# Kernel optimization log

Hardware: AMD Instinct MI355X
Metric: run time of the kernel (lower is better)

## Reference

```python
import jax, jax.numpy as jnp
import numpy as np

B, S, H, D = 2, 2048, 32, 128


def setup_inputs() -> dict:
    key = jax.random.key(0)
    qkv = jax.random.normal(key, (B, S, 3, H, D), dtype=jnp.float32)
    return {"qkv": qkv, "causal": 1}


def reference(qkv, causal):
    # qkv: [B, S, 3, H, D] packed as in flash_attn qkvpacked convention.
    # Distributed all-to-all / ring rotation is identity math on one device,
    # so this is standard scaled-dot-product attention.
    q = qkv[:, :, 0]  # [B, S, H, D]
    k = qkv[:, :, 1]
    v = qkv[:, :, 2]
    scale = 1.0 / jnp.sqrt(jnp.asarray(q.shape[-1], q.dtype))
    # [B, H, S, S]
    logits = jnp.einsum("bshd,bthd->bhst", q, k) * scale
    if causal:
        s = q.shape[1]
        mask = jnp.tril(jnp.ones((s, s), dtype=bool))  # [S, S]
        logits = jnp.where(mask[None, None], logits, jnp.finfo(logits.dtype).min)
    probs = jax.nn.softmax(logits, axis=-1)
    out = jnp.einsum("bhst,bthd->bshd", probs, v)  # [B, S, H, D]
    return out
```

## Files before the change

### kernel.cpp

```cpp
#include <hip/hip_runtime.h>
#include <hip/hip_bf16.h>

constexpr int Bc = 2;
constexpr int Sc = 2048;
constexpr int Hc = 32;
constexpr int Dc = 128;
constexpr int QKV_STRIDE = 3 * Hc * Dc;

constexpr int BQ = 128;
constexpr int BK = 64;
constexpr float SCALE_LOG2E = 0.088388347648318f * 1.442695040888963f;
constexpr float DEFER_THR = 8.0f;

constexpr int KST = 132;
constexpr int VST = 68;

typedef __attribute__((ext_vector_type(8)))  short    bf16x8;
typedef __attribute__((ext_vector_type(4)))  short    bf16x4;
typedef __attribute__((ext_vector_type(16))) float    f32x16;
typedef __attribute__((ext_vector_type(4)))  unsigned u32x4;

static __device__ __forceinline__ short f2bf(float f) {
    __bf16 h = (__bf16)f;
    return __builtin_bit_cast(short, h);
}
static __device__ __forceinline__ unsigned pk2(float lo, float hi) {
    union { short2 s; unsigned u; } x;
    x.s.x = f2bf(lo); x.s.y = f2bf(hi);
    return x.u;
}
static __device__ __forceinline__ void plswap(unsigned& dst, unsigned& src) {
    asm volatile("v_permlane32_swap_b32 %0, %1" : "+v"(dst), "+v"(src));
}
static __device__ __forceinline__ void lds_barrier() {
    asm volatile("s_waitcnt lgkmcnt(0)" ::: "memory");
    __builtin_amdgcn_s_barrier();
    asm volatile("" ::: "memory");
}

__global__ __launch_bounds__(256)
void attn_fwd(const float* __restrict__ qkv,
              const int* __restrict__ causal_p,
              float* __restrict__ out)
{
    const int bid = blockIdx.x;
    const int o   = bid >> 6;
    const int bh  = bid & 63;
    const int r_  = o & 3;
    const int j_  = o >> 2;
    const int bq_ = 15 - 2 * r_;
    const int qt  = (j_ < 2) ? (bq_ - j_) : (15 - bq_ + 3 - j_);

    const int b = bh >> 5;
    const int h = bh & 31;
    const int causal = *causal_p;

    const int tid  = threadIdx.x;
    const int w    = tid >> 6;
    const int lane = tid & 63;
    const int l31  = lane & 31;
    const int hf   = lane >> 5;

    __shared__ short Ks[64 * KST];
    __shared__ short Vs[128 * VST];

    const int q0  = qt * BQ;
    const int wq0 = q0 + w * 32;

    const int kg = tid >> 5;
    const int dl = tid & 31;

    const float* kplane = qkv + (size_t)b * Sc * QKV_STRIDE + Hc * Dc + h * Dc;

    bf16x8 qf[8];
    {
        const float* qb = qkv + (size_t)(b * Sc + wq0 + l31) * QKV_STRIDE + h * Dc;
        #pragma unroll
        for (int st = 0; st < 8; ++st) {
            const float* p = qb + st * 16 + hf * 8;
            float4 x0 = *(const float4*)(p);
            float4 x1 = *(const float4*)(p + 4);
            bf16x8 q;
            q[0] = f2bf(x0.x * SCALE_LOG2E);
            q[1] = f2bf(x0.y * SCALE_LOG2E);
            q[2] = f2bf(x0.z * SCALE_LOG2E);
            q[3] = f2bf(x0.w * SCALE_LOG2E);
            q[4] = f2bf(x1.x * SCALE_LOG2E);
            q[5] = f2bf(x1.y * SCALE_LOG2E);
            q[6] = f2bf(x1.z * SCALE_LOG2E);
            q[7] = f2bf(x1.w * SCALE_LOG2E);
            qf[st] = q;
        }
    }

    f32x16 o_[4];
    #pragma unroll
    for (int db = 0; db < 4; ++db)
        #pragma unroll
        for (int i = 0; i < 16; ++i) o_[db][i] = 0.f;
    float m = -1e30f, l = 0.f;

    const int nkv = causal ? (2 * qt + 2) : (Sc / BK);

    float4 kst[8];
    float  vst[8][4];

    auto issue = [&](int kt) {
        const float* kb = kplane + (size_t)(kt * BK + kg * 8) * QKV_STRIDE;
        #pragma unroll
        for (int j = 0; j < 8; ++j)
            kst[j] = *(const float4*)(kb + (size_t)j * QKV_STRIDE + dl * 4);
        const float* vb = kb + Hc * Dc;
        #pragma unroll
        for (int j = 0; j < 8; ++j) {
            #pragma unroll
            for (int q = 0; q < 4; ++q)
                vst[j][q] = vb[(size_t)j * QKV_STRIDE + q * 32 + dl];
        }
    };

    auto commit = [&]() {
        #pragma unroll
        for (int j = 0; j < 8; ++j) {
            bf16x4 kk;
            kk[0] = f2bf(kst[j].x); kk[1] = f2bf(kst[j].y);
            kk[2] = f2bf(kst[j].z); kk[3] = f2bf(kst[j].w);
            *(bf16x4*)&Ks[(kg * 8 + j) * KST + dl * 4] = kk;
        }
        #pragma unroll
        for (int q = 0; q < 4; ++q) {
            bf16x8 vv;
            #pragma unroll
            for (int j = 0; j < 8; ++j) vv[j] = f2bf(vst[j][q]);
            *(bf16x8*)&Vs[(q * 32 + dl) * VST + kg * 8] = vv;
        }
    };

    issue(0);

    for (int kt = 0; kt < nkv; ++kt) {
        lds_barrier();
        commit();
        if (kt + 1 < nkv) issue(kt + 1);
        lds_barrier();

        const int kbase = kt * BK;
        if (causal && kbase > wq0 + 31) continue;

        f32x16 acc[2];
        #pragma unroll
        for (int mb = 0; mb < 2; ++mb)
            #pragma unroll
            for (int i = 0; i < 16; ++i) acc[mb][i] = 0.f;
        __builtin_amdgcn_s_setprio(1);
        #pragma unroll
        for (int st = 0; st < 8; ++st) {
            #pragma unroll
            for (int mb = 0; mb < 2; ++mb) {
                bf16x8 ka = *(const bf16x8*)&Ks[(mb * 32 + l31) * KST + st * 16 + hf * 8];
                acc[mb] = __builtin_amdgcn_mfma_f32_32x32x16_bf16(ka, qf[st], acc[mb], 0, 0, 0);
            }
        }
        __builtin_amdgcn_s_setprio(0);

        if (causal && kbase + 63 > wq0) {
            const int qg = wq0 + l31;
            #pragma unroll
            for (int mb = 0; mb < 2; ++mb) {
                #pragma unroll
                for (int r = 0; r < 16; ++r) {
                    const int kgl = kbase + mb * 32 + (r & 3) + 8 * (r >> 2) + 4 * hf;
                    if (kgl > qg) acc[mb][r] = -1e30f;
                }
            }
        }

        float pm = acc[0][0];
        #pragma unroll
        for (int i = 1; i < 16; ++i) pm = fmaxf(pm, acc[0][i]);
        #pragma unroll
        for (int i = 0; i < 16; ++i) pm = fmaxf(pm, acc[1][i]);
        pm = fmaxf(pm, __shfl_xor(pm, 32));
        if (__any(pm > m + DEFER_THR)) {
            const float mnew  = fmaxf(m, pm);
            const float alpha = __builtin_amdgcn_exp2f(m - mnew);
            m = mnew; l *= alpha;
            #pragma unroll
            for (int r = 0; r < 16; ++r) {
                const float ar = __shfl(alpha, (r & 3) + 8 * (r >> 2) + 4 * hf);
                o_[0][r] *= ar; o_[1][r] *= ar; o_[2][r] *= ar; o_[3][r] *= ar;
            }
        }
        float rs = 0.f;
        #pragma unroll
        for (int i = 0; i < 16; ++i) {
            const float p = __builtin_amdgcn_exp2f(acc[0][i] - m);
            acc[0][i] = p; rs += p;
        }
        #pragma unroll
        for (int i = 0; i < 16; ++i) {
            const float p = __builtin_amdgcn_exp2f(acc[1][i] - m);
            acc[1][i] = p; rs += p;
        }
        rs += __shfl_xor(rs, 32);
        l += rs;

        unsigned wpk[2][4][2];
        #pragma unroll
        for (int mb = 0; mb < 2; ++mb)
            #pragma unroll
            for (int c = 0; c < 4; ++c) {
                wpk[mb][c][0] = pk2(acc[mb][4 * c + 0], acc[mb][4 * c + 1]);
                wpk[mb][c][1] = pk2(acc[mb][4 * c + 2], acc[mb][4 * c + 3]);
            }
        bf16x8 pa[4];
        #pragma unroll
        for (int ks = 0; ks < 4; ++ks) {
            const int mb = ks >> 1, ci = ks & 1;
            unsigned e0 = wpk[mb][2 * ci][0], o0 = wpk[mb][2 * ci + 1][0];
            unsigned e1 = wpk[mb][2 * ci][1], o1 = wpk[mb][2 * ci + 1][1];
            plswap(e0, o0);
            plswap(e1, o1);
            u32x4 wv;
            wv[0] = e0; wv[1] = e1; wv[2] = o0; wv[3] = o1;
            pa[ks] = __builtin_bit_cast(bf16x8, wv);
        }

        __builtin_amdgcn_s_setprio(1);
        #pragma unroll
        for (int ks = 0; ks < 4; ++ks) {
            #pragma unroll
            for (int db = 0; db < 4; ++db) {
                bf16x8 vb = *(const bf16x8*)&Vs[(db * 32 + l31) * VST + ks * 16 + hf * 8];
                o_[db] = __builtin_amdgcn_mfma_f32_32x32x16_bf16(pa[ks], vb, o_[db], 0, 0, 0);
            }
        }
        __builtin_amdgcn_s_setprio(0);
    }

    #pragma unroll
    for (int r = 0; r < 16; ++r) {
        const int rq = (r & 3) + 8 * (r >> 2) + 4 * hf;
        const float lr = __shfl(l, rq);
        const float inv = 1.f / lr;
        const int qg = wq0 + rq;
        float* ob = out + (size_t)(b * Sc + qg) * (Hc * Dc) + h * Dc + l31;
        ob[0]  = o_[0][r] * inv;
        ob[32] = o_[1][r] * inv;
        ob[64] = o_[2][r] * inv;
        ob[96] = o_[3][r] * inv;
    }
}

extern "C" void kernel_launch(void* const* d_in, const int* in_sizes, int n_in,
                              void* d_out, int out_size, void* d_ws, size_t ws_size,
                              hipStream_t stream) {
    const float* qkv = (const float*)d_in[0];
    const int* causal = (const int*)d_in[1];
    float* out = (float*)d_out;
    dim3 grid((Sc / BQ) * Bc * Hc);
    attn_fwd<<<grid, 256, 0, stream>>>(qkv, causal, out);
}
```

Measured before the change: 197.1 us.

## Double-buffer K/V shared tiles to overlap staging with compute

Splits shared memory into two K/V buffers and unrolls the KV loop by two. While the current tile is consumed by QK^T, softmax and PV, the next tile's prefetched registers are converted and written into the other buffer. This cuts the barriers per tile from two to one and hides the LDS commit behind MFMA work. The cost is twice the LDS footprint, which lowers the number of resident blocks per CU, plus more code and possibly more register pressure.

```diff
diff --git a/kernel.cpp b/kernel.cpp
--- a/kernel.cpp
+++ b/kernel.cpp
@@ -61,8 +61,8 @@
     const int l31  = lane & 31;
     const int hf   = lane >> 5;
 
-    __shared__ short Ks[64 * KST];
-    __shared__ short Vs[128 * VST];
+    __shared__ short KsA[64 * KST], KsB[64 * KST];
+    __shared__ short VsA[128 * VST], VsB[128 * VST];
 
     const int q0  = qt * BQ;
     const int wq0 = q0 + w * 32;
@@ -119,35 +119,24 @@
         }
     };
 
-    auto commit = [&]() {
+    auto commit = [&](short* ksp, short* vsp) {
         #pragma unroll
         for (int j = 0; j < 8; ++j) {
             bf16x4 kk;
             kk[0] = f2bf(kst[j].x); kk[1] = f2bf(kst[j].y);
             kk[2] = f2bf(kst[j].z); kk[3] = f2bf(kst[j].w);
-            *(bf16x4*)&Ks[(kg * 8 + j) * KST + dl * 4] = kk;
+            *(bf16x4*)&ksp[(kg * 8 + j) * KST + dl * 4] = kk;
         }
         #pragma unroll
         for (int q = 0; q < 4; ++q) {
             bf16x8 vv;
             #pragma unroll
             for (int j = 0; j < 8; ++j) vv[j] = f2bf(vst[j][q]);
-            *(bf16x8*)&Vs[(q * 32 + dl) * VST + kg * 8] = vv;
-        }
-    };
-
-    issue(0);
-
-    for (int kt = 0; kt < nkv; ++kt) {
-        lds_barrier();
-        commit();
-        if (kt + 1 < nkv) issue(kt + 1);
-        lds_barrier();
-
-        const int kbase = kt * BK;
-        if (causal && kbase > wq0 + 31) continue;
-
-        f32x16 acc[2];
+            *(bf16x8*)&vsp[(q * 32 + dl) * VST + kg * 8] = vv;
+        }
+    };
+
+    auto qk_phase = [&](const short* ksp, f32x16* acc) {
         #pragma unroll
         for (int mb = 0; mb < 2; ++mb)
             #pragma unroll
@@ -157,12 +146,14 @@
         for (int st = 0; st < 8; ++st) {
             #pragma unroll
             for (int mb = 0; mb < 2; ++mb) {
-                bf16x8 ka = *(const bf16x8*)&Ks[(mb * 32 + l31) * KST + st * 16 + hf * 8];
+                bf16x8 ka = *(const bf16x8*)&ksp[(mb * 32 + l31) * KST + st * 16 + hf * 8];
                 acc[mb] = __builtin_amdgcn_mfma_f32_32x32x16_bf16(ka, qf[st], acc[mb], 0, 0, 0);
             }
         }
         __builtin_amdgcn_s_setprio(0);
-
+    };
+
+    auto sm_pv_phase = [&](int kbase, f32x16* acc, const short* vsp) {
         if (causal && kbase + 63 > wq0) {
             const int qg = wq0 + l31;
             #pragma unroll
@@ -231,11 +222,40 @@
         for (int ks = 0; ks < 4; ++ks) {
             #pragma unroll
             for (int db = 0; db < 4; ++db) {
-                bf16x8 vb = *(const bf16x8*)&Vs[(db * 32 + l31) * VST + ks * 16 + hf * 8];
+                bf16x8 vb = *(const bf16x8*)&vsp[(db * 32 + l31) * VST + ks * 16 + hf * 8];
                 o_[db] = __builtin_amdgcn_mfma_f32_32x32x16_bf16(pa[ks], vb, o_[db], 0, 0, 0);
             }
         }
         __builtin_amdgcn_s_setprio(0);
+    };
+
+    issue(0);
+    commit(KsA, VsA);
+    issue(1);
+    lds_barrier();
+
+    for (int kt = 0; kt < nkv; kt += 2) {
+        {
+            const int kbase = kt * BK;
+            const bool skip = causal && kbase > wq0 + 31;
+            f32x16 acc[2];
+            if (!skip) qk_phase(KsA, acc);
+            commit(KsB, VsB);
+            if (kt + 2 < nkv) issue(kt + 2);
+            if (!skip) sm_pv_phase(kbase, acc, VsA);
+        }
+        lds_barrier();
+
+        {
+            const int kbase = (kt + 1) * BK;
+            const bool skip = causal && kbase > wq0 + 31;
+            f32x16 acc[2];
+            if (!skip) qk_phase(KsB, acc);
+            if (kt + 2 < nkv) commit(KsA, VsA);
+            if (kt + 3 < nkv) issue(kt + 3);
+            if (!skip) sm_pv_phase(kbase, acc, VsB);
+        }
+        lds_barrier();
     }
 
     #pragma unroll
```

Result: slower. 401.3 us (+103.6%).

## Pre-convert K/V to bf16 LDS images in workspace and stream via direct-to-LDS loads

Applied to the files above, without the earlier changes.

Adds a pre-pass kernel that converts each 64-row K/V tile to bf16 and writes it in the exact padded LDS layout (K row-major, V transposed) into the workspace. The attention kernel then copies each tile straight into LDS with global_load_lds, instead of strided fp32 loads followed by per-thread conversion, which removes redundant conversion work and halves the bytes read per tile. The cost is an extra kernel launch plus a workspace write and read. The main loop also loses its register prefetch and waits on vmcnt(0) right after each copy, so load latency is no longer overlapped with compute. The old kernel is kept as a fallback for when the workspace is too small.

```diff
diff --git a/kernel.cpp b/kernel.cpp
--- a/kernel.cpp
+++ b/kernel.cpp
@@ -15,10 +15,15 @@
 constexpr int KST = 132;
 constexpr int VST = 68;
 
+constexpr int V_OFF = 64 * KST * 2;
+constexpr int IMGB  = 36864;
+constexpr size_t WS_NEED = (size_t)Bc * Hc * (Sc / BK) * IMGB;
+
 typedef __attribute__((ext_vector_type(8)))  short    bf16x8;
 typedef __attribute__((ext_vector_type(4)))  short    bf16x4;
 typedef __attribute__((ext_vector_type(16))) float    f32x16;
 typedef __attribute__((ext_vector_type(4)))  unsigned u32x4;
+typedef unsigned int u32;
 
 static __device__ __forceinline__ short f2bf(float f) {
     __bf16 h = (__bf16)f;
@@ -37,11 +42,68 @@
     __builtin_amdgcn_s_barrier();
     asm volatile("" ::: "memory");
 }
+static __device__ __forceinline__ void glds16(const char* g, char* l) {
+    __builtin_amdgcn_global_load_lds(
+        (const __attribute__((address_space(1))) u32*)g,
+        (__attribute__((address_space(3))) u32*)l, 16, 0, 0);
+}
 
 __global__ __launch_bounds__(256)
-void attn_fwd(const float* __restrict__ qkv,
-              const int* __restrict__ causal_p,
-              float* __restrict__ out)
+void preconv(const float* __restrict__ qkv, char* __restrict__ ws)
+{
+    const int bid = blockIdx.x;
+    const int bh = bid >> 5, kt = bid & 31;
+    const int b = bh >> 5, h = bh & 31;
+    char* img = ws + (size_t)bid * IMGB;
+
+    const int t  = threadIdx.x;
+    const int r  = t >> 2;
+    const int cq = (t & 3) * 32;
+
+    const float* kro = qkv + (size_t)(b * Sc + kt * 64 + r) * QKV_STRIDE
+                       + Hc * Dc + h * Dc + cq;
+    {
+        short* kout = (short*)img + r * KST + cq;
+        #pragma unroll
+        for (int v = 0; v < 4; ++v) {
+            float4 a = *(const float4*)(kro + v * 8);
+            float4 c = *(const float4*)(kro + v * 8 + 4);
+            bf16x8 pk;
+            pk[0] = f2bf(a.x); pk[1] = f2bf(a.y); pk[2] = f2bf(a.z); pk[3] = f2bf(a.w);
+            pk[4] = f2bf(c.x); pk[5] = f2bf(c.y); pk[6] = f2bf(c.z); pk[7] = f2bf(c.w);
+            *(bf16x8*)(kout + v * 8) = pk;
+        }
+    }
+    __shared__ float vt[64 * 129];
+    {
+        const float* vro = kro + Hc * Dc;
+        #pragma unroll
+        for (int v = 0; v < 8; ++v) {
+            float4 a = *(const float4*)(vro + v * 4);
+            float* dst = &vt[r * 129 + cq + v * 4];
+            dst[0] = a.x; dst[1] = a.y; dst[2] = a.z; dst[3] = a.w;
+        }
+    }
+    __syncthreads();
+    {
+        const int d = t >> 1, half = t & 1;
+        short* vout = (short*)(img + V_OFF) + d * VST + half * 32;
+        #pragma unroll
+        for (int v = 0; v < 4; ++v) {
+            bf16x8 pk;
+            #pragma unroll
+            for (int j = 0; j < 8; ++j)
+                pk[j] = f2bf(vt[(half * 32 + v * 8 + j) * 129 + d]);
+            *(bf16x8*)(vout + v * 8) = pk;
+        }
+    }
+}
+
+__global__ __launch_bounds__(256)
+void attn_ws(const char* __restrict__ ws,
+             const int* __restrict__ causal_p,
+             const float* __restrict__ qkv,
+             float* __restrict__ out)
 {
     const int bid = blockIdx.x;
     const int o   = bid >> 6;
@@ -61,16 +123,14 @@
     const int l31  = lane & 31;
     const int hf   = lane >> 5;
 
-    __shared__ short Ks[64 * KST];
-    __shared__ short Vs[128 * VST];
+    __shared__ char lbuf[IMGB];
+    short* Ks = (short*)lbuf;
+    short* Vs = (short*)(lbuf + V_OFF);
 
     const int q0  = qt * BQ;
     const int wq0 = q0 + w * 32;
 
-    const int kg = tid >> 5;
-    const int dl = tid & 31;
-
-    const float* kplane = qkv + (size_t)b * Sc * QKV_STRIDE + Hc * Dc + h * Dc;
+    const char* imgs = ws + (size_t)bh * 32 * IMGB;
 
     bf16x8 qf[8];
     {
@@ -102,46 +162,16 @@
 
     const int nkv = causal ? (2 * qt + 2) : (Sc / BK);
 
-    float4 kst[8];
-    float  vst[8][4];
-
-    auto issue = [&](int kt) {
-        const float* kb = kplane + (size_t)(kt * BK + kg * 8) * QKV_STRIDE;
-        #pragma unroll
-        for (int j = 0; j < 8; ++j)
-            kst[j] = *(const float4*)(kb + (size_t)j * QKV_STRIDE + dl * 4);
-        const float* vb = kb + Hc * Dc;
-        #pragma unroll
-        for (int j = 0; j < 8; ++j) {
-            #pragma unroll
-            for (int q = 0; q < 4; ++q)
-                vst[j][q] = vb[(size_t)j * QKV_STRIDE + q * 32 + dl];
-        }
-    };
-
-    auto commit = [&]() {
-        #pragma unroll
-        for (int j = 0; j < 8; ++j) {
-            bf16x4 kk;
-            kk[0] = f2bf(kst[j].x); kk[1] = f2bf(kst[j].y);
-            kk[2] = f2bf(kst[j].z); kk[3] = f2bf(kst[j].w);
-            *(bf16x4*)&Ks[(kg * 8 + j) * KST + dl * 4] = kk;
-        }
-        #pragma unroll
-        for (int q = 0; q < 4; ++q) {
-            bf16x8 vv;
-            #pragma unroll
-            for (int j = 0; j < 8; ++j) vv[j] = f2bf(vst[j][q]);
-            *(bf16x8*)&Vs[(q * 32 + dl) * VST + kg * 8] = vv;
-        }
-    };
-
-    issue(0);
-
     for (int kt = 0; kt < nkv; ++kt) {
         lds_barrier();
-        commit();
-        if (kt + 1 < nkv) issue(kt + 1);
+        {
+            const char* src = imgs + (size_t)kt * IMGB + w * 9216 + lane * 16;
+            char* dst = lbuf + w * 9216;
+            #pragma unroll
+            for (int i = 0; i < 9; ++i)
+                glds16(src + i * 1024, dst + i * 1024);
+        }
+        asm volatile("s_waitcnt vmcnt(0)" ::: "memory");
         lds_barrier();
 
         const int kbase = kt * BK;
@@ -252,12 +282,226 @@
     }
 }
 
+__global__ __launch_bounds__(256)
+void attn_fb(const float* __restrict__ qkv,
+             const int* __restrict__ causal_p,
+             float* __restrict__ out)
+{
+    const int bid = blockIdx.x;
+    const int o   = bid >> 6;
+    const int bh  = bid & 63;
+    const int r_  = o & 3;
+    const int j_  = o >> 2;
+    const int bq_ = 15 - 2 * r_;
+    const int qt  = (j_ < 2) ? (bq_ - j_) : (15 - bq_ + 3 - j_);
+
+    const int b = bh >> 5;
+    const int h = bh & 31;
+    const int causal = *causal_p;
+
+    const int tid  = threadIdx.x;
+    const int w    = tid >> 6;
+    const int lane = tid & 63;
+    const int l31  = lane & 31;
+    const int hf   = lane >> 5;
+
+    __shared__ short Ks[64 * KST];
+    __shared__ short Vs[128 * VST];
+
+    const int q0  = qt * BQ;
+    const int wq0 = q0 + w * 32;
+    const int kg = tid >> 5;
+    const int dl = tid & 31;
+
+    const float* kplane = qkv + (size_t)b * Sc * QKV_STRIDE + Hc * Dc + h * Dc;
+
+    bf16x8 qf[8];
+    {
+        const float* qb = qkv + (size_t)(b * Sc + wq0 + l31) * QKV_STRIDE + h * Dc;
+        #pragma unroll
+        for (int st = 0; st < 8; ++st) {
+            const float* p = qb + st * 16 + hf * 8;
+            float4 x0 = *(const float4*)(p);
+            float4 x1 = *(const float4*)(p + 4);
+            bf16x8 q;
+            q[0] = f2bf(x0.x * SCALE_LOG2E);
+            q[1] = f2bf(x0.y * SCALE_LOG2E);
+            q[2] = f2bf(x0.z * SCALE_LOG2E);
+            q[3] = f2bf(x0.w * SCALE_LOG2E);
+            q[4] = f2bf(x1.x * SCALE_LOG2E);
+            q[5] = f2bf(x1.y * SCALE_LOG2E);
+            q[6] = f2bf(x1.z * SCALE_LOG2E);
+            q[7] = f2bf(x1.w * SCALE_LOG2E);
+            qf[st] = q;
+        }
+    }
+
+    f32x16 o_[4];
+    #pragma unroll
+    for (int db = 0; db < 4; ++db)
+        #pragma unroll
+        for (int i = 0; i < 16; ++i) o_[db][i] = 0.f;
+    float m = -1e30f, l = 0.f;
+
+    const int nkv = causal ? (2 * qt + 2) : (Sc / BK);
+    float4 kst[8];
+    float  vst[8][4];
+
+    auto issue = [&](int kt) {
+        const float* kb = kplane + (size_t)(kt * BK + kg * 8) * QKV_STRIDE;
+        #pragma unroll
+        for (int j = 0; j < 8; ++j)
+            kst[j] = *(const float4*)(kb + (size_t)j * QKV_STRIDE + dl * 4);
+        const float* vb = kb + Hc * Dc;
+        #pragma unroll
+        for (int j = 0; j < 8; ++j) {
+            #pragma unroll
+            for (int q = 0; q < 4; ++q)
+                vst[j][q] = vb[(size_t)j * QKV_STRIDE + q * 32 + dl];
+        }
+    };
+    auto commit = [&]() {
+        #pragma unroll
+        for (int j = 0; j < 8; ++j) {
+            bf16x4 kk;
+            kk[0] = f2bf(kst[j].x); kk[1] = f2bf(kst[j].y);
+            kk[2] = f2bf(kst[j].z); kk[3] = f2bf(kst[j].w);
+            *(bf16x4*)&Ks[(kg * 8 + j) * KST + dl * 4] = kk;
+        }
+        #pragma unroll
+        for (int q = 0; q < 4; ++q) {
+            bf16x8 vv;
+            #pragma unroll
+            for (int j = 0; j < 8; ++j) vv[j] = f2bf(vst[j][q]);
+            *(bf16x8*)&Vs[(q * 32 + dl) * VST + kg * 8] = vv;
+        }
+    };
+
+    issue(0);
+    for (int kt = 0; kt < nkv; ++kt) {
+        lds_barrier();
+        commit();
+        if (kt + 1 < nkv) issue(kt + 1);
+        lds_barrier();
+
+        const int kbase = kt * BK;
+        if (causal && kbase > wq0 + 31) continue;
+
+        f32x16 acc[2];
+        #pragma unroll
+        for (int mb = 0; mb < 2; ++mb)
+            #pragma unroll
+            for (int i = 0; i < 16; ++i) acc[mb][i] = 0.f;
+        __builtin_amdgcn_s_setprio(1);
+        #pragma unroll
+        for (int st = 0; st < 8; ++st) {
+            #pragma unroll
+            for (int mb = 0; mb < 2; ++mb) {
+                bf16x8 ka = *(const bf16x8*)&Ks[(mb * 32 + l31) * KST + st * 16 + hf * 8];
+                acc[mb] = __builtin_amdgcn_mfma_f32_32x32x16_bf16(ka, qf[st], acc[mb], 0, 0, 0);
+            }
+        }
+        __builtin_amdgcn_s_setprio(0);
+
+        if (causal && kbase + 63 > wq0) {
+            const int qg = wq0 + l31;
+            #pragma unroll
+            for (int mb = 0; mb < 2; ++mb) {
+                #pragma unroll
+                for (int r = 0; r < 16; ++r) {
+                    const int kgl = kbase + mb * 32 + (r & 3) + 8 * (r >> 2) + 4 * hf;
+                    if (kgl > qg) acc[mb][r] = -1e30f;
+                }
+            }
+        }
+
+        float pm = acc[0][0];
+        #pragma unroll
+        for (int i = 1; i < 16; ++i) pm = fmaxf(pm, acc[0][i]);
+        #pragma unroll
+        for (int i = 0; i < 16; ++i) pm = fmaxf(pm, acc[1][i]);
+        pm = fmaxf(pm, __shfl_xor(pm, 32));
+        if (__any(pm > m + DEFER_THR)) {
+            const float mnew  = fmaxf(m, pm);
+            const float alpha = __builtin_amdgcn_exp2f(m - mnew);
+            m = mnew; l *= alpha;
+            #pragma unroll
+            for (int r = 0; r < 16; ++r) {
+                const float ar = __shfl(alpha, (r & 3) + 8 * (r >> 2) + 4 * hf);
+                o_[0][r] *= ar; o_[1][r] *= ar; o_[2][r] *= ar; o_[3][r] *= ar;
+            }
+        }
+        float rs = 0.f;
+        #pragma unroll
+        for (int i = 0; i < 16; ++i) {
+            const float p = __builtin_amdgcn_exp2f(acc[0][i] - m);
+            acc[0][i] = p; rs += p;
+        }
+        #pragma unroll
+        for (int i = 0; i < 16; ++i) {
+            const float p = __builtin_amdgcn_exp2f(acc[1][i] - m);
+            acc[1][i] = p; rs += p;
+        }
+        rs += __shfl_xor(rs, 32);
+        l += rs;
+
+        unsigned wpk[2][4][2];
+        #pragma unroll
+        for (int mb = 0; mb < 2; ++mb)
+            #pragma unroll
+            for (int c = 0; c < 4; ++c) {
+                wpk[mb][c][0] = pk2(acc[mb][4 * c + 0], acc[mb][4 * c + 1]);
+                wpk[mb][c][1] = pk2(acc[mb][4 * c + 2], acc[mb][4 * c + 3]);
+            }
+        bf16x8 pa[4];
+        #pragma unroll
+        for (int ks = 0; ks < 4; ++ks) {
+            const int mb = ks >> 1, ci = ks & 1;
+            unsigned e0 = wpk[mb][2 * ci][0], o0 = wpk[mb][2 * ci + 1][0];
+            unsigned e1 = wpk[mb][2 * ci][1], o1 = wpk[mb][2 * ci + 1][1];
+            plswap(e0, o0);
+            plswap(e1, o1);
+            u32x4 wv;
+            wv[0] = e0; wv[1] = e1; wv[2] = o0; wv[3] = o1;
+            pa[ks] = __builtin_bit_cast(bf16x8, wv);
+        }
+
+        __builtin_amdgcn_s_setprio(1);
+        #pragma unroll
+        for (int ks = 0; ks < 4; ++ks) {
+            #pragma unroll
+            for (int db = 0; db < 4; ++db) {
+                bf16x8 vb = *(const bf16x8*)&Vs[(db * 32 + l31) * VST + ks * 16 + hf * 8];
+                o_[db] = __builtin_amdgcn_mfma_f32_32x32x16_bf16(pa[ks], vb, o_[db], 0, 0, 0);
+            }
+        }
+        __builtin_amdgcn_s_setprio(0);
+    }
+
+    #pragma unroll
+    for (int r = 0; r < 16; ++r) {
+        const int rq = (r & 3) + 8 * (r >> 2) + 4 * hf;
+        const float lr = __shfl(l, rq);
+        const float inv = 1.f / lr;
+        const int qg = wq0 + rq;
+        float* ob = out + (size_t)(b * Sc + qg) * (Hc * Dc) + h * Dc + l31;
+        ob[0]  = o_[0][r] * inv;
+        ob[32] = o_[1][r] * inv;
+        ob[64] = o_[2][r] * inv;
+        ob[96] = o_[3][r] * inv;
+    }
+}
+
 extern "C" void kernel_launch(void* const* d_in, const int* in_sizes, int n_in,
                               void* d_out, int out_size, void* d_ws, size_t ws_size,
                               hipStream_t stream) {
     const float* qkv = (const float*)d_in[0];
     const int* causal = (const int*)d_in[1];
     float* out = (float*)d_out;
-    dim3 grid((Sc / BQ) * Bc * Hc);
-    attn_fwd<<<grid, 256, 0, stream>>>(qkv, causal, out);
-}
+    if (ws_size >= WS_NEED) {
+        preconv<<<Bc * Hc * (Sc / BK), 256, 0, stream>>>(qkv, (char*)d_ws);
+        attn_ws<<<(Sc / BQ) * Bc * Hc, 256, 0, stream>>>((const char*)d_ws, causal, qkv, out);
+    } else {
+        attn_fb<<<(Sc / BQ) * Bc * Hc, 256, 0, stream>>>(qkv, causal, out);
+    }
+}
```

Measured after the change: 437.0 us. +121.8%, slower.

## Double-buffer K/V LDS tiles and prefetch V fragments into registers

Applied to the files above, without the earlier changes.

Replaces the single K/V LDS buffer with two ping-pong buffers, so the bf16 conversion and store of the next tile overlaps with compute on the current tile, and the global loads are issued two tiles ahead. This cuts the per-iteration barriers from two to one. V fragments are loaded into registers right after QK^T, before the commit, which keeps the ordering correct. The cost is twice the LDS, which may reduce occupancy, plus 16 extra bf16x8 registers of pressure and a deeper register-staged prefetch.

```diff
diff --git a/kernel.cpp b/kernel.cpp
--- a/kernel.cpp
+++ b/kernel.cpp
@@ -14,6 +14,8 @@
 
 constexpr int KST = 132;
 constexpr int VST = 68;
+constexpr int KSH = 64 * KST;
+constexpr int BUFSH = KSH + 128 * VST;
 
 typedef __attribute__((ext_vector_type(8)))  short    bf16x8;
 typedef __attribute__((ext_vector_type(4)))  short    bf16x4;
@@ -61,8 +63,7 @@
     const int l31  = lane & 31;
     const int hf   = lane >> 5;
 
-    __shared__ short Ks[64 * KST];
-    __shared__ short Vs[128 * VST];
+    __shared__ short lds2[2 * BUFSH];
 
     const int q0  = qt * BQ;
     const int wq0 = q0 + w * 32;
@@ -119,123 +120,145 @@
         }
     };
 
-    auto commit = [&]() {
+    auto commit = [&](short* ksp, short* vsp) {
         #pragma unroll
         for (int j = 0; j < 8; ++j) {
             bf16x4 kk;
             kk[0] = f2bf(kst[j].x); kk[1] = f2bf(kst[j].y);
             kk[2] = f2bf(kst[j].z); kk[3] = f2bf(kst[j].w);
-            *(bf16x4*)&Ks[(kg * 8 + j) * KST + dl * 4] = kk;
+            *(bf16x4*)&ksp[(kg * 8 + j) * KST + dl * 4] = kk;
         }
         #pragma unroll
         for (int q = 0; q < 4; ++q) {
             bf16x8 vv;
             #pragma unroll
             for (int j = 0; j < 8; ++j) vv[j] = f2bf(vst[j][q]);
-            *(bf16x8*)&Vs[(q * 32 + dl) * VST + kg * 8] = vv;
+            *(bf16x8*)&vsp[(q * 32 + dl) * VST + kg * 8] = vv;
         }
     };
 
     issue(0);
+    commit(&lds2[0], &lds2[KSH]);
+    issue(1);
+    lds_barrier();
 
     for (int kt = 0; kt < nkv; ++kt) {
+        const int cur = kt & 1;
+        short* Ksb = &lds2[cur * BUFSH];
+        short* Vsb = Ksb + KSH;
+        short* Ksn = &lds2[(cur ^ 1) * BUFSH];
+        short* Vsn = Ksn + KSH;
+
+        const int kbase = kt * BK;
+        const bool active = !(causal && kbase > wq0 + 31);
+
+        f32x16 acc[2];
+        bf16x8 vreg[16];
+
+        if (active) {
+            #pragma unroll
+            for (int mb = 0; mb < 2; ++mb)
+                #pragma unroll
+                for (int i = 0; i < 16; ++i) acc[mb][i] = 0.f;
+            __builtin_amdgcn_s_setprio(1);
+            #pragma unroll
+            for (int st = 0; st < 8; ++st) {
+                #pragma unroll
+                for (int mb = 0; mb < 2; ++mb) {
+                    bf16x8 ka = *(const bf16x8*)&Ksb[(mb * 32 + l31) * KST + st * 16 + hf * 8];
+                    acc[mb] = __builtin_amdgcn_mfma_f32_32x32x16_bf16(ka, qf[st], acc[mb], 0, 0, 0);
+                }
+            }
+            __builtin_amdgcn_s_setprio(0);
+            #pragma unroll
+            for (int ks = 0; ks < 4; ++ks)
+                #pragma unroll
+                for (int db = 0; db < 4; ++db)
+                    vreg[ks * 4 + db] =
+                        *(const bf16x8*)&Vsb[(db * 32 + l31) * VST + ks * 16 + hf * 8];
+        }
+
+        __builtin_amdgcn_sched_barrier(0);
+
+        if (kt + 1 < nkv) commit(Ksn, Vsn);
+        if (kt + 2 < nkv) issue(kt + 2);
+
+        if (active) {
+            if (causal && kbase + 63 > wq0) {
+                const int qg = wq0 + l31;
+                #pragma unroll
+                for (int mb = 0; mb < 2; ++mb) {
+                    #pragma unroll
+                    for (int r = 0; r < 16; ++r) {
+                        const int kgl = kbase + mb * 32 + (r & 3) + 8 * (r >> 2) + 4 * hf;
+                        if (kgl > qg) acc[mb][r] = -1e30f;
+                    }
+                }
+            }
+
+            float pm = acc[0][0];
+            #pragma unroll
+            for (int i = 1; i < 16; ++i) pm = fmaxf(pm, acc[0][i]);
+            #pragma unroll
+            for (int i = 0; i < 16; ++i) pm = fmaxf(pm, acc[1][i]);
+            pm = fmaxf(pm, __shfl_xor(pm, 32));
+            if (__any(pm > m + DEFER_THR)) {
+                const float mnew  = fmaxf(m, pm);
+                const float alpha = __builtin_amdgcn_exp2f(m - mnew);
+                m = mnew; l *= alpha;
+                #pragma unroll
+                for (int r = 0; r < 16; ++r) {
+                    const float ar = __shfl(alpha, (r & 3) + 8 * (r >> 2) + 4 * hf);
+                    o_[0][r] *= ar; o_[1][r] *= ar; o_[2][r] *= ar; o_[3][r] *= ar;
+                }
+            }
+            float rs = 0.f;
+            #pragma unroll
+            for (int i = 0; i < 16; ++i) {
+                const float p = __builtin_amdgcn_exp2f(acc[0][i] - m);
+                acc[0][i] = p; rs += p;
+            }
+            #pragma unroll
+            for (int i = 0; i < 16; ++i) {
+                const float p = __builtin_amdgcn_exp2f(acc[1][i] - m);
+                acc[1][i] = p; rs += p;
+            }
+            rs += __shfl_xor(rs, 32);
+            l += rs;
+
+            unsigned wpk[2][4][2];
+            #pragma unroll
+            for (int mb = 0; mb < 2; ++mb)
+                #pragma unroll
+                for (int c = 0; c < 4; ++c) {
+                    wpk[mb][c][0] = pk2(acc[mb][4 * c + 0], acc[mb][4 * c + 1]);
+                    wpk[mb][c][1] = pk2(acc[mb][4 * c + 2], acc[mb][4 * c + 3]);
+                }
+            bf16x8 pa[4];
+            #pragma unroll
+            for (int ks = 0; ks < 4; ++ks) {
+                const int mb = ks >> 1, ci = ks & 1;
+                unsigned e0 = wpk[mb][2 * ci][0], o0 = wpk[mb][2 * ci + 1][0];
+                unsigned e1 = wpk[mb][2 * ci][1], o1 = wpk[mb][2 * ci + 1][1];
+                plswap(e0, o0);
+                plswap(e1, o1);
+                u32x4 wv;
+                wv[0] = e0; wv[1] = e1; wv[2] = o0; wv[3] = o1;
+                pa[ks] = __builtin_bit_cast(bf16x8, wv);
+            }
+
+            __builtin_amdgcn_s_setprio(1);
+            #pragma unroll
+            for (int ks = 0; ks < 4; ++ks) {
+                #pragma unroll
+                for (int db = 0; db < 4; ++db)
+                    o_[db] = __builtin_amdgcn_mfma_f32_32x32x16_bf16(
+                        pa[ks], vreg[ks * 4 + db], o_[db], 0, 0, 0);
+            }
+            __builtin_amdgcn_s_setprio(0);
+        }
+
         lds_barrier();
-        commit();
-        if (kt + 1 < nkv) issue(kt + 1);
-        lds_barrier();
-
-        const int kbase = kt * BK;
-        if (causal && kbase > wq0 + 31) continue;
-
-        f32x16 acc[2];
-        #pragma unroll
-        for (int mb = 0; mb < 2; ++mb)
-            #pragma unroll
-            for (int i = 0; i < 16; ++i) acc[mb][i] = 0.f;
-        __builtin_amdgcn_s_setprio(1);
-        #pragma unroll
-        for (int st = 0; st < 8; ++st) {
-            #pragma unroll
-            for (int mb = 0; mb < 2; ++mb) {
-                bf16x8 ka = *(const bf16x8*)&Ks[(mb * 32 + l31) * KST + st * 16 + hf * 8];
-                acc[mb] = __builtin_amdgcn_mfma_f32_32x32x16_bf16(ka, qf[st], acc[mb], 0, 0, 0);
-            }
-        }
-        __builtin_amdgcn_s_setprio(0);
-
-        if (causal && kbase + 63 > wq0) {
-            const int qg = wq0 + l31;
-            #pragma unroll
-            for (int mb = 0; mb < 2; ++mb) {
-                #pragma unroll
-                for (int r = 0; r < 16; ++r) {
-                    const int kgl = kbase + mb * 32 + (r & 3) + 8 * (r >> 2) + 4 * hf;
-                    if (kgl > qg) acc[mb][r] = -1e30f;
-                }
-            }
-        }
-
-        float pm = acc[0][0];
-        #pragma unroll
-        for (int i = 1; i < 16; ++i) pm = fmaxf(pm, acc[0][i]);
-        #pragma unroll
-        for (int i = 0; i < 16; ++i) pm = fmaxf(pm, acc[1][i]);
-        pm = fmaxf(pm, __shfl_xor(pm, 32));
-        if (__any(pm > m + DEFER_THR)) {
-            const float mnew  = fmaxf(m, pm);
-            const float alpha = __builtin_amdgcn_exp2f(m - mnew);
-            m = mnew; l *= alpha;
-            #pragma unroll
-            for (int r = 0; r < 16; ++r) {
-                const float ar = __shfl(alpha, (r & 3) + 8 * (r >> 2) + 4 * hf);
-                o_[0][r] *= ar; o_[1][r] *= ar; o_[2][r] *= ar; o_[3][r] *= ar;
-            }
-        }
-        float rs = 0.f;
-        #pragma unroll
-        for (int i = 0; i < 16; ++i) {
-            const float p = __builtin_amdgcn_exp2f(acc[0][i] - m);
-            acc[0][i] = p; rs += p;
-        }
-        #pragma unroll
-        for (int i = 0; i < 16; ++i) {
-            const float p = __builtin_amdgcn_exp2f(acc[1][i] - m);
-            acc[1][i] = p; rs += p;
-        }
-        rs += __shfl_xor(rs, 32);
-        l += rs;
-
-        unsigned wpk[2][4][2];
-        #pragma unroll
-        for (int mb = 0; mb < 2; ++mb)
-            #pragma unroll
-            for (int c = 0; c < 4; ++c) {
-                wpk[mb][c][0] = pk2(acc[mb][4 * c + 0], acc[mb][4 * c + 1]);
-                wpk[mb][c][1] = pk2(acc[mb][4 * c + 2], acc[mb][4 * c + 3]);
-            }
-        bf16x8 pa[4];
-        #pragma unroll
-        for (int ks = 0; ks < 4; ++ks) {
-            const int mb = ks >> 1, ci = ks & 1;
-            unsigned e0 = wpk[mb][2 * ci][0], o0 = wpk[mb][2 * ci + 1][0];
-            unsigned e1 = wpk[mb][2 * ci][1], o1 = wpk[mb][2 * ci + 1][1];
-            plswap(e0, o0);
-            plswap(e1, o1);
-            u32x4 wv;
-            wv[0] = e0; wv[1] = e1; wv[2] = o0; wv[3] = o1;
-            pa[ks] = __builtin_bit_cast(bf16x8, wv);
-        }
-
-        __builtin_amdgcn_s_setprio(1);
-        #pragma unroll
-        for (int ks = 0; ks < 4; ++ks) {
-            #pragma unroll
-            for (int db = 0; db < 4; ++db) {
-                bf16x8 vb = *(const bf16x8*)&Vs[(db * 32 + l31) * VST + ks * 16 + hf * 8];
-                o_[db] = __builtin_amdgcn_mfma_f32_32x32x16_bf16(pa[ks], vb, o_[db], 0, 0, 0);
-            }
-        }
-        __builtin_amdgcn_s_setprio(0);
     }
 
     #pragma unroll
```

After: 432.9 us. 2.2x slower.
